# Optimization experiments

Hardware: AMD Instinct MI355X
Metric: run time of the kernel (lower is better)

The kernel has to match this reference:

```python
import jax, jax.numpy as jnp
import numpy as np

BN_EPS = 1e-5
KS = 4  # 4x4 morphology kernel (np.ones((4,4)))


def _bn(x, gamma, beta, mean, var):
    # eval-mode BatchNorm2d over channel dim 1 of [B,C,H,W]
    inv = jax.lax.rsqrt(var + BN_EPS)
    return (x - mean[None, :, None, None]) * (gamma * inv)[None, :, None, None] + beta[None, :, None, None]


def _erosion_to_dilate(m):
    # m: [B,1,H,W]; threshold > 0.3, then 4x4 binary erosion (min-pool) and
    # dilation (max-pool), SAME padding; border padded so it does not erode/dilate,
    # matching cv2's default morphology border behavior.
    z = jnp.where(m > 0.3, 1.0, 0.0).astype(m.dtype)
    er = jax.lax.reduce_window(z, jnp.array(1.0, z.dtype), jax.lax.min,
                               (1, 1, KS, KS), (1, 1, 1, 1), 'SAME')
    di = jax.lax.reduce_window(z, jnp.array(0.0, z.dtype), jax.lax.max,
                               (1, 1, KS, KS), (1, 1, 1, 1), 'SAME')
    # [maske, background, maskd] along channel dim -> [B,3,H,W]
    return jnp.concatenate([er, 1.0 - di, di - er], axis=1)


def setup_inputs() -> dict:
    key = jax.random.key(0)
    ks = jax.random.split(key, 8)
    B, C, H, W = 8, 256, 128, 128
    feature = jax.random.normal(ks[0], (B, C, H, W), dtype=jnp.float32)
    m = jax.random.uniform(ks[1], (B, 1, H, W), dtype=jnp.float32)
    w_feat = jax.random.normal(ks[2], (C, C), dtype=jnp.float32) * 0.02
    w_out = jax.random.normal(ks[3], (C, 2 * C), dtype=jnp.float32) * 0.02
    bn_f_gamma = jnp.ones((C,), jnp.float32)
    bn_f_beta = jnp.zeros((C,), jnp.float32)
    bn_f_mean = jnp.zeros((C,), jnp.float32)
    bn_f_var = jnp.ones((C,), jnp.float32)
    bn_o_gamma = jnp.ones((C,), jnp.float32)
    bn_o_beta = jnp.zeros((C,), jnp.float32)
    bn_o_mean = jnp.zeros((C,), jnp.float32)
    bn_o_var = jnp.ones((C,), jnp.float32)
    return {"feature": feature, "m": m, "w_feat": w_feat,
            "bn_f_gamma": bn_f_gamma, "bn_f_beta": bn_f_beta,
            "bn_f_mean": bn_f_mean, "bn_f_var": bn_f_var,
            "w_out": w_out, "bn_o_gamma": bn_o_gamma, "bn_o_beta": bn_o_beta,
            "bn_o_mean": bn_o_mean, "bn_o_var": bn_o_var}


def reference(feature, m, w_feat, bn_f_gamma, bn_f_beta, bn_f_mean, bn_f_var,
              w_out, bn_o_gamma, bn_o_beta, bn_o_mean, bn_o_var):
    B, C, H, W = feature.shape
    HW = H * W
    m = jax.nn.relu(m)
    # erosion_to_dilate is computed via numpy/OpenCV in the original -> detached
    fbu = jax.lax.stop_gradient(_erosion_to_dilate(m)).reshape(B, 3, HW)
    f1 = feature.reshape(B, C, HW)
    # mid_feature = fbu @ feature^T : [B,3,C]
    mid = jnp.einsum('bkn,bcn->bkc', fbu, f1)
    # conv1x1_feature: 1x1 conv (no bias) + eval BN, NO relu (BasicConv2d.forward)
    cf = _bn(jnp.einsum('bchw,oc->bohw', feature, w_feat),
             bn_f_gamma, bn_f_beta, bn_f_mean, bn_f_var).reshape(B, C, HW)
    mid1 = jnp.einsum('bkc,bcn->bkn', mid, cf)          # [B,3,HW]
    mid2 = jnp.einsum('bkc,bkn->bcn', mid, mid1)        # [B,C,HW]
    mid2 = mid2.reshape(B, C, H, W)
    cat = jnp.concatenate([feature, mid2], axis=1)      # [B,2C,H,W]
    out = _bn(jnp.einsum('bchw,oc->bohw', cat, w_out),
              bn_o_gamma, bn_o_beta, bn_o_mean, bn_o_var)
    return out
```

## Files before the change

kernel.cpp:

```cpp
#include <hip/hip_runtime.h>

#define HW 16384
#define TP 72

typedef unsigned short ushort_t;
typedef unsigned int uint32;
typedef __attribute__((ext_vector_type(8))) short short8;
typedef __attribute__((ext_vector_type(4))) ushort_t ushortx4;
typedef __attribute__((ext_vector_type(4))) float floatx4;

__device__ __forceinline__ ushort_t f2bf(float x) {
  uint32 u = __float_as_uint(x);
  u += 0x7fffu + ((u >> 16) & 1u);
  return (ushort_t)(u >> 16);
}

__global__ __launch_bounds__(256) void k_masks(const float* __restrict__ m,
                                               float* __restrict__ er,
                                               float* __restrict__ di) {
  int idx = blockIdx.x * 256 + threadIdx.x;
  int b = idx >> 14;
  int p = idx & (HW - 1);
  int i = p >> 7, j = p & 127;
  const float* mb = m + (b << 14);
  float ermn = 1.f, dimx = 0.f;
  for (int di_ = -1; di_ <= 2; ++di_) {
    int ii = i + di_;
    if (ii < 0 || ii >= 128) continue;
    for (int dj = -1; dj <= 2; ++dj) {
      int jj = j + dj;
      if (jj < 0 || jj >= 128) continue;
      float z = ((double)mb[ii * 128 + jj] > 0.3) ? 1.f : 0.f;
      ermn = fminf(ermn, z);
      dimx = fmaxf(dimx, z);
    }
  }
  er[idx] = ermn;
  di[idx] = dimx;
}

__global__ __launch_bounds__(256) void k_midsums(const float* __restrict__ f,
                                                 const float* __restrict__ er,
                                                 const float* __restrict__ di,
                                                 float* __restrict__ out,
                                                 ushort_t* __restrict__ fbf) {
  int b = blockIdx.x >> 8;
  int c = blockIdx.x & 255;
  const size_t chan = (size_t)(b * 256 + c) << 14;
  const float4* f4 = (const float4*)(f + chan);
  const float4* e4 = (const float4*)(er + ((size_t)b << 14));
  const float4* d4 = (const float4*)(di + ((size_t)b << 14));
  ushort_t* fb = fbf + chan;
  int t = threadIdx.x;
  float se = 0.f, st = 0.f, sd = 0.f;
#pragma unroll
  for (int it = 0; it < 16; ++it) {
    int i = it * 256 + t;
    float4 x = f4[i];
    float4 e = e4[i];
    float4 dd = d4[i];
    st += (x.x + x.y) + (x.z + x.w);
    se += x.x * e.x + x.y * e.y + x.z * e.z + x.w * e.w;
    sd += x.x * dd.x + x.y * dd.y + x.z * dd.z + x.w * dd.w;
    ushortx4 pv;
    pv[0] = f2bf(x.x); pv[1] = f2bf(x.y); pv[2] = f2bf(x.z); pv[3] = f2bf(x.w);
    *(ushortx4*)(fb + (size_t)i * 4) = pv;
  }
  __shared__ float red[3][4];
  for (int off = 32; off; off >>= 1) {
    se += __shfl_down(se, off);
    st += __shfl_down(st, off);
    sd += __shfl_down(sd, off);
  }
  int wave = t >> 6;
  if ((t & 63) == 0) { red[0][wave] = se; red[1][wave] = st; red[2][wave] = sd; }
  __syncthreads();
  if (t == 0) {
    se = red[0][0] + red[0][1] + red[0][2] + red[0][3];
    st = red[1][0] + red[1][1] + red[1][2] + red[1][3];
    sd = red[2][0] + red[2][1] + red[2][2] + red[2][3];
    float* o = out + (size_t)(b * 256 + c) * 3;
    o[0] = se; o[1] = st; o[2] = sd;
  }
}

__global__ __launch_bounds__(1024) void k_prep_a(
    const float* __restrict__ midsums, const float* __restrict__ wfeat,
    const float* __restrict__ gf, const float* __restrict__ bfp,
    const float* __restrict__ mfp, const float* __restrict__ vfp,
    const float* __restrict__ wout, const float* __restrict__ g2,
    const float* __restrict__ b2p, const float* __restrict__ m2p,
    const float* __restrict__ v2p, float* __restrict__ BmW,
    float* __restrict__ A2W, float* __restrict__ bias_eff) {
  const int b = blockIdx.x;
  const int tid = threadIdx.x;
  const int t = tid & 255;
  const int part = tid >> 8;
  __shared__ float mid[3][256];
  __shared__ float msc[3][256];
  __shared__ float tl[256];
  __shared__ float s2l[256], t2l[256];
  __shared__ float bias2[256];
  __shared__ float ulp[3][4];
  __shared__ float ul[3];
  __shared__ float Bmp[4][3][256];
  __shared__ float A2p[4][256][3];
  __shared__ float bbp[4][256];

  if (part == 0) {
    const float* ms = midsums + (size_t)(b * 256 + t) * 3;
    float se = ms[0], st = ms[1], sd = ms[2];
    float m0 = se, m1 = st - sd, m2v = sd - se;
    mid[0][t] = m0; mid[1][t] = m1; mid[2][t] = m2v;
    float s = gf[t] * rsqrtf(vfp[t] + 1e-5f);
    tl[t] = bfp[t] - mfp[t] * s;
    msc[0][t] = m0 * s; msc[1][t] = m1 * s; msc[2][t] = m2v * s;
    float s2 = g2[t] * rsqrtf(v2p[t] + 1e-5f);
    s2l[t] = s2;
    t2l[t] = b2p[t] - m2p[t] * s2;
  }
  __syncthreads();
  if (t < 3) {
    float u = 0.f;
#pragma unroll 8
    for (int c = part * 64; c < part * 64 + 64; ++c) u += mid[t][c] * tl[c];
    ulp[t][part] = u;
  }
  {
    float b0 = 0.f, b1 = 0.f, b2v = 0.f;
#pragma unroll 8
    for (int o = part * 64; o < part * 64 + 64; ++o) {
      float wfv = wfeat[o * 256 + t];
      b0 += msc[0][o] * wfv;
      b1 += msc[1][o] * wfv;
      b2v += msc[2][o] * wfv;
    }
    Bmp[part][0][t] = b0; Bmp[part][1][t] = b1; Bmp[part][2][t] = b2v;
  }
  __syncthreads();
  if (tid < 3) ul[tid] = ulp[tid][0] + ulp[tid][1] + ulp[tid][2] + ulp[tid][3];
  if (part == 0) {
#pragma unroll
    for (int k = 0; k < 3; ++k)
      BmW[b * 768 + k * 256 + t] =
          Bmp[0][k][t] + Bmp[1][k][t] + Bmp[2][k][t] + Bmp[3][k][t];
  }
  __syncthreads();
  if (part == 0) bias2[t] = mid[0][t] * ul[0] + mid[1][t] * ul[1] + mid[2][t] * ul[2];
  __syncthreads();
  {
    const float4* w2 = (const float4*)(wout + t * 512 + 256);
    float a0 = 0.f, a1 = 0.f, a2v = 0.f, bb = 0.f;
#pragma unroll 4
    for (int cq = part * 16; cq < part * 16 + 16; ++cq) {
      float4 wv = w2[cq];
      int c = cq * 4;
      a0 += wv.x * mid[0][c] + wv.y * mid[0][c + 1] + wv.z * mid[0][c + 2] + wv.w * mid[0][c + 3];
      a1 += wv.x * mid[1][c] + wv.y * mid[1][c + 1] + wv.z * mid[1][c + 2] + wv.w * mid[1][c + 3];
      a2v += wv.x * mid[2][c] + wv.y * mid[2][c + 1] + wv.z * mid[2][c + 2] + wv.w * mid[2][c + 3];
      bb += wv.x * bias2[c] + wv.y * bias2[c + 1] + wv.z * bias2[c + 2] + wv.w * bias2[c + 3];
    }
    A2p[part][t][0] = a0; A2p[part][t][1] = a1; A2p[part][t][2] = a2v;
    bbp[part][t] = bb;
  }
  __syncthreads();
  if (part == 0) {
#pragma unroll
    for (int k = 0; k < 3; ++k)
      A2W[(size_t)(b * 256 + t) * 3 + k] =
          A2p[0][t][k] + A2p[1][t][k] + A2p[2][t][k] + A2p[3][t][k];
    float bb = bbp[0][t] + bbp[1][t] + bbp[2][t] + bbp[3][t];
    bias_eff[b * 256 + t] = s2l[t] * bb + t2l[t];
  }
}

__global__ __launch_bounds__(256) void k_wbuild(
    const float* __restrict__ wout, const float* __restrict__ g2,
    const float* __restrict__ v2p, const float* __restrict__ BmW,
    const float* __restrict__ A2W, ushort_t* __restrict__ Wbf) {
  const int b = blockIdx.x >> 5;
  const int og = blockIdx.x & 31;
  const int t = threadIdx.x;
  __shared__ float s2o[8];
  __shared__ float a2s[8][3];
  float bm0 = BmW[b * 768 + t];
  float bm1 = BmW[b * 768 + 256 + t];
  float bm2 = BmW[b * 768 + 512 + t];
  if (t < 8) {
    int o = og * 8 + t;
    s2o[t] = g2[o] * rsqrtf(v2p[o] + 1e-5f);
  }
  if (t < 24) {
    int i = t / 3, k = t % 3;
    a2s[i][k] = A2W[(size_t)(b * 256 + og * 8 + i) * 3 + k];
  }
  __syncthreads();
  ushort_t* Wb = Wbf + ((size_t)b << 16);
#pragma unroll
  for (int i = 0; i < 8; ++i) {
    int o = og * 8 + i;
    float wv = wout[o * 512 + t];
    float val = s2o[i] * (wv + a2s[i][0] * bm0 + a2s[i][1] * bm1 + a2s[i][2] * bm2);
    Wb[o * 256 + t] = f2bf(val);
  }
}

__global__ __launch_bounds__(256) void k_gemm(const ushort_t* __restrict__ fbf,
                                              const ushort_t* __restrict__ Wbf,
                                              const float* __restrict__ bias,
                                              float* __restrict__ out) {
  __shared__ __align__(16) ushort_t ldsT[64 * TP];
  const int b = blockIdx.x >> 8;
  const int n0 = (blockIdx.x & 255) * 64;
  const int t = threadIdx.x;
  const int wv = t >> 6;
  const int lane = t & 63;
  const int l15 = lane & 15;
  const int quad = lane >> 4;
  const int obase = wv * 64;
  const ushort_t* fb = fbf + ((size_t)b << 22);
  const ushort_t* Wb = Wbf + ((size_t)b << 16);
  const float* biasb = bias + (b << 8);

  const int c_loc = t >> 2;
  const int nb = t & 3;

  floatx4 acc[4][4];
#pragma unroll
  for (int ot = 0; ot < 4; ++ot) {
#pragma unroll
    for (int r = 0; r < 4; ++r) {
      float bv = biasb[obase + ot * 16 + quad * 4 + r];
#pragma unroll
      for (int nt = 0; nt < 4; ++nt) acc[ot][nt][r] = bv;
    }
  }

  for (int kc = 0; kc < 256; kc += 64) {
    const ushort_t* gsrc = fb + (size_t)(kc + c_loc) * HW + n0 + nb * 16;
    short8 v0 = *(const short8*)(gsrc);
    short8 v1 = *(const short8*)(gsrc + 8);
    if (kc) __syncthreads();
    ushort_t* dst = ldsT + c_loc;
#pragma unroll
    for (int j = 0; j < 8; ++j) {
      dst[(nb * 16 + j) * TP] = (ushort_t)v0[j];
      dst[(nb * 16 + 8 + j) * TP] = (ushort_t)v1[j];
    }
    __syncthreads();
#pragma unroll
    for (int ks = 0; ks < 2; ++ks) {
      short8 a[4];
#pragma unroll
      for (int ot = 0; ot < 4; ++ot)
        a[ot] = *(const short8*)(Wb + (size_t)(obase + ot * 16 + l15) * 256 +
                                 kc + ks * 32 + quad * 8);
      short8 bfr[4];
#pragma unroll
      for (int nt = 0; nt < 4; ++nt)
        bfr[nt] = *(const short8*)(ldsT + (nt * 16 + l15) * TP + ks * 32 + quad * 8);
#pragma unroll
      for (int ot = 0; ot < 4; ++ot)
#pragma unroll
        for (int nt = 0; nt < 4; ++nt)
          acc[ot][nt] = __builtin_amdgcn_mfma_f32_16x16x32_bf16(a[ot], bfr[nt], acc[ot][nt], 0, 0, 0);
    }
  }

  float* ob = out + ((size_t)b << 22);
#pragma unroll
  for (int ot = 0; ot < 4; ++ot)
#pragma unroll
    for (int nt = 0; nt < 4; ++nt)
#pragma unroll
      for (int r = 0; r < 4; ++r)
        ob[(size_t)(obase + ot * 16 + quad * 4 + r) * HW + n0 + nt * 16 + l15] = acc[ot][nt][r];
}

extern "C" void kernel_launch(void* const* d_in, const int* in_sizes, int n_in,
                              void* d_out, int out_size, void* d_ws, size_t ws_size,
                              hipStream_t stream) {
  (void)in_sizes; (void)n_in; (void)out_size; (void)ws_size;
  const float* feature = (const float*)d_in[0];
  const float* m = (const float*)d_in[1];
  const float* w_feat = (const float*)d_in[2];
  const float* gf = (const float*)d_in[3];
  const float* bf = (const float*)d_in[4];
  const float* mf = (const float*)d_in[5];
  const float* vf = (const float*)d_in[6];
  const float* w_out = (const float*)d_in[7];
  const float* g2 = (const float*)d_in[8];
  const float* b2 = (const float*)d_in[9];
  const float* m2 = (const float*)d_in[10];
  const float* v2 = (const float*)d_in[11];
  float* out = (float*)d_out;

  char* wsb = (char*)d_ws;
  float* er = (float*)wsb;
  float* di = (float*)(wsb + (512 << 10));
  float* midsums = (float*)(wsb + (1 << 20));
  float* bias_eff = (float*)(wsb + (1 << 20) + (32 << 10));
  float* BmW = (float*)(wsb + (1 << 20) + (64 << 10));
  float* A2W = (float*)(wsb + (1 << 20) + (128 << 10));
  ushort_t* Wbf = (ushort_t*)(wsb + (2 << 20));
  ushort_t* fbf = (ushort_t*)(wsb + (4 << 20));

  hipLaunchKernelGGL(k_masks, dim3(512), dim3(256), 0, stream, m, er, di);
  hipLaunchKernelGGL(k_midsums, dim3(2048), dim3(256), 0, stream, feature, er, di, midsums, fbf);
  hipLaunchKernelGGL(k_prep_a, dim3(8), dim3(1024), 0, stream, midsums, w_feat,
                     gf, bf, mf, vf, w_out, g2, b2, m2, v2, BmW, A2W, bias_eff);
  hipLaunchKernelGGL(k_wbuild, dim3(256), dim3(256), 0, stream, w_out, g2, v2, BmW, A2W, Wbf);
  hipLaunchKernelGGL(k_gemm, dim3(2048), dim3(256), 0, stream, fbf, Wbf, bias_eff, out);
}
```

Measured before the change: 317.9 us.

## Double-buffer LDS tiles in GEMM and prefetch next K chunk during MFMA

The GEMM kernel now keeps two LDS buffers. It issues the global loads for the next 64-channel chunk before running the MFMAs on the current chunk, then writes the prefetched data into the other buffer, which leaves one barrier per iteration instead of two. The LDS layout also pads each 16-column group with a GP stride, meant to reduce bank conflicts on the transposed stores. The cost is twice the LDS and extra registers to hold the prefetched vectors, which may reduce occupancy.

Result: no change. 319.4 us (+0.5%).

```diff
diff --git a/kernel.cpp b/kernel.cpp
--- a/kernel.cpp
+++ b/kernel.cpp
@@ -2,6 +2,8 @@
 
 #define HW 16384
 #define TP 72
+#define GP 1168
+#define BUFSZ 4672
 
 typedef unsigned short ushort_t;
 typedef unsigned int uint32;
@@ -209,7 +211,7 @@
                                               const ushort_t* __restrict__ Wbf,
                                               const float* __restrict__ bias,
                                               float* __restrict__ out) {
-  __shared__ __align__(16) ushort_t ldsT[64 * TP];
+  __shared__ __align__(16) ushort_t ldsT[2 * BUFSZ];
   const int b = blockIdx.x >> 8;
   const int n0 = (blockIdx.x & 255) * 64;
   const int t = threadIdx.x;
@@ -236,34 +238,54 @@
     }
   }
 
-  for (int kc = 0; kc < 256; kc += 64) {
-    const ushort_t* gsrc = fb + (size_t)(kc + c_loc) * HW + n0 + nb * 16;
+  {
+    const ushort_t* gsrc = fb + (size_t)c_loc * HW + n0 + nb * 16;
     short8 v0 = *(const short8*)(gsrc);
     short8 v1 = *(const short8*)(gsrc + 8);
-    if (kc) __syncthreads();
-    ushort_t* dst = ldsT + c_loc;
+    ushort_t* dst = ldsT + nb * GP + c_loc;
 #pragma unroll
     for (int j = 0; j < 8; ++j) {
-      dst[(nb * 16 + j) * TP] = (ushort_t)v0[j];
-      dst[(nb * 16 + 8 + j) * TP] = (ushort_t)v1[j];
-    }
-    __syncthreads();
+      dst[j * TP] = (ushort_t)v0[j];
+      dst[(8 + j) * TP] = (ushort_t)v1[j];
+    }
+  }
+  __syncthreads();
+
+#pragma unroll
+  for (int kct = 0; kct < 4; ++kct) {
+    const int cur = kct & 1;
+    short8 w0, w1;
+    if (kct < 3) {
+      const ushort_t* gsrc = fb + (size_t)((kct + 1) * 64 + c_loc) * HW + n0 + nb * 16;
+      w0 = *(const short8*)(gsrc);
+      w1 = *(const short8*)(gsrc + 8);
+    }
+    const ushort_t* bufr = ldsT + cur * BUFSZ;
 #pragma unroll
     for (int ks = 0; ks < 2; ++ks) {
       short8 a[4];
 #pragma unroll
       for (int ot = 0; ot < 4; ++ot)
         a[ot] = *(const short8*)(Wb + (size_t)(obase + ot * 16 + l15) * 256 +
-                                 kc + ks * 32 + quad * 8);
+                                 kct * 64 + ks * 32 + quad * 8);
       short8 bfr[4];
 #pragma unroll
       for (int nt = 0; nt < 4; ++nt)
-        bfr[nt] = *(const short8*)(ldsT + (nt * 16 + l15) * TP + ks * 32 + quad * 8);
+        bfr[nt] = *(const short8*)(bufr + nt * GP + l15 * TP + ks * 32 + quad * 8);
 #pragma unroll
       for (int ot = 0; ot < 4; ++ot)
 #pragma unroll
         for (int nt = 0; nt < 4; ++nt)
           acc[ot][nt] = __builtin_amdgcn_mfma_f32_16x16x32_bf16(a[ot], bfr[nt], acc[ot][nt], 0, 0, 0);
+    }
+    if (kct < 3) {
+      ushort_t* dst = ldsT + (cur ^ 1) * BUFSZ + nb * GP + c_loc;
+#pragma unroll
+      for (int j = 0; j < 8; ++j) {
+        dst[j * TP] = (ushort_t)w0[j];
+        dst[(8 + j) * TP] = (ushort_t)w1[j];
+      }
+      __syncthreads();
     }
   }
 
```
